# Kernel optimization log

Hardware: AMD Instinct MI355X
Metric: run time of the kernel (lower is better)

## Reference

```python
import jax, jax.numpy as jnp
import numpy as np

N_NODES = 100000
N_EDGES = 1600000
N_GRAPHS = 64
F = 128  # feature_dim == hidden_dim == embedding_dim
NUM_CONVS = 3


def _layernorm(h, g, b, eps=1e-5):
    mu = jnp.mean(h, axis=-1, keepdims=True)
    var = jnp.var(h, axis=-1, keepdims=True)
    return (h - mu) * jax.lax.rsqrt(var + eps) * g + b


def setup_inputs() -> dict:
    key = jax.random.key(0)
    ks = jax.random.split(key, 12)
    s = 1.0 / np.sqrt(F)
    return {
        "x": jax.random.normal(ks[0], (N_NODES, F), jnp.float32),
        "edge_index": jax.random.randint(ks[1], (2, N_EDGES), 0, N_NODES, jnp.int32),
        "batch_vec": jnp.sort(jax.random.randint(ks[2], (N_NODES,), 0, N_GRAPHS, jnp.int32)),
        "gammas": 1.0 + 0.1 * jax.random.normal(ks[3], (N_GRAPHS, NUM_CONVS), jnp.float32),
        "betas": 0.1 * jax.random.normal(ks[4], (N_GRAPHS, NUM_CONVS), jnp.float32),
        "pre_W0": s * jax.random.normal(ks[5], (F, F), jnp.float32),
        "pre_b0": jnp.zeros((F,), jnp.float32),
        "pre_W1": s * jax.random.normal(ks[6], (F, F), jnp.float32),
        "pre_b1": jnp.zeros((F,), jnp.float32),
        "gin_W": s * jax.random.normal(ks[7], (NUM_CONVS, 2, F, F), jnp.float32),
        "gin_b": jnp.zeros((NUM_CONVS, 2, F), jnp.float32),
        "post_W0": (1.0 / np.sqrt(5 * F)) * jax.random.normal(ks[8], (5 * F, F), jnp.float32),
        "post_b0": jnp.zeros((F,), jnp.float32),
        "post_ln_g": jnp.ones((F,), jnp.float32),
        "post_ln_b": jnp.zeros((F,), jnp.float32),
        "post_W1": s * jax.random.normal(ks[9], (F, F), jnp.float32),
        "post_b1": jnp.zeros((F,), jnp.float32),
    }


def reference(x, edge_index, batch_vec, gammas, betas,
              pre_W0, pre_b0, pre_W1, pre_b1,
              gin_W, gin_b,
              post_W0, post_b0, post_ln_g, post_ln_b, post_W1, post_b1):
    n = x.shape[0]
    src, dst = edge_index[0], edge_index[1]

    # preprocess MLP (2 layers, ReLU between, batch_norm='none')
    h = jnp.dot(jax.nn.relu(jnp.dot(x, pre_W0) + pre_b0), pre_W1) + pre_b1
    jump_xs = [x, h]

    # per-node FiLM coefficients (repeat_interleave over sorted batch == gather)
    g_nodes = gammas[batch_vec]  # [N, num_convs]
    b_nodes = betas[batch_vec]   # [N, num_convs]

    for i in range(NUM_CONVS):
        # GINConv, eps=0: MLP(h_i + sum_{j->i} h_j)
        aggr = jax.ops.segment_sum(h[src], dst, num_segments=n)
        z = h + aggr
        h = jnp.dot(jax.nn.relu(jnp.dot(z, gin_W[i, 0]) + gin_b[i, 0]), gin_W[i, 1]) + gin_b[i, 1]
        # FiLM modulation
        h = h * g_nodes[:, i:i + 1] + b_nodes[:, i:i + 1]
        jump_xs.append(h)

    # jumping knowledge 'cat'
    h = jnp.concatenate(jump_xs, axis=-1)  # [N, feature + 4*hidden]

    # postprocess MLP with LayerNorm (batch_norm='layer'); dropout p=0 (eval)
    z = jnp.dot(h, post_W0) + post_b0
    z = jax.nn.relu(_layernorm(z, post_ln_g, post_ln_b))
    return jnp.dot(z, post_W1) + post_b1
```

## Files before the change

### kernel.cpp

```cpp
#include <hip/hip_runtime.h>
#include <stdint.h>

#define FDIM 128
constexpr int EP_NONE = 0, EP_RELU = 1, EP_FILM = 2, EP_LNRELU = 3;

typedef __attribute__((ext_vector_type(8))) short short8v;
typedef __attribute__((ext_vector_type(4))) float f32x4;

struct Srcs { const float* p[5]; };
struct WPtrs { const float* p[14]; };

__device__ inline short f2bf(float f) {
  unsigned u = __float_as_uint(f);
  u = (u + 0x7fffu + ((u >> 16) & 1u)) >> 16;
  return (short)u;
}
__device__ inline float bf2f(short s) {
  return __uint_as_float(((unsigned)(unsigned short)s) << 16);
}


__global__ __launch_bounds__(256)
void k_hist(const int* __restrict__ dst, int* __restrict__ cnt, int E) {
  int e = blockIdx.x * 256 + threadIdx.x;
  if (e < E) atomicAdd(&cnt[dst[e]], 1);
}

__global__ __launch_bounds__(1024)
void k_scan_block(const int* __restrict__ cnt, int* __restrict__ scanned,
                  int* __restrict__ partials, int n) {
  __shared__ int sd[1024];
  int tid = threadIdx.x;
  int i = blockIdx.x * 1024 + tid;
  int v = (i < n) ? cnt[i] : 0;
  sd[tid] = v; __syncthreads();
  for (int off = 1; off < 1024; off <<= 1) {
    int t = (tid >= off) ? sd[tid - off] : 0;
    __syncthreads();
    sd[tid] += t;
    __syncthreads();
  }
  if (i < n) scanned[i] = sd[tid] - v;
  if (tid == 1023) partials[blockIdx.x] = sd[1023];
}

__global__ __launch_bounds__(128)
void k_scan_small(const int* __restrict__ partials, int* __restrict__ p2, int nb) {
  __shared__ int sd[128];
  int tid = threadIdx.x;
  int v = (tid < nb) ? partials[tid] : 0;
  sd[tid] = v; __syncthreads();
  for (int off = 1; off < 128; off <<= 1) {
    int t = (tid >= off) ? sd[tid - off] : 0;
    __syncthreads();
    sd[tid] += t;
    __syncthreads();
  }
  p2[tid] = sd[tid] - v;
}

__global__ __launch_bounds__(256)
void k_finalize(const int* __restrict__ scanned, const int* __restrict__ p2,
                int* __restrict__ indptr, int* __restrict__ cursor, int n, int E) {
  int i = blockIdx.x * 256 + threadIdx.x;
  if (i < n) {
    int v = scanned[i] + p2[i >> 10];
    indptr[i] = v;
    cursor[i] = v;
  }
  if (i == 0) indptr[n] = E;
}

__global__ __launch_bounds__(256)
void k_scatter(const int* __restrict__ src, const int* __restrict__ dst,
               int* __restrict__ cursor, int* __restrict__ eids, int E) {
  int e = blockIdx.x * 256 + threadIdx.x;
  if (e < E) {
    int p = atomicAdd(&cursor[dst[e]], 1);
    eids[p] = src[e];
  }
}


__global__ __launch_bounds__(256)
void k_aggr(const float* __restrict__ h, const int* __restrict__ indptr,
            const int* __restrict__ eids, float* __restrict__ z, int n) {
  int lane = threadIdx.x & 63;
  int node = blockIdx.x * 4 + (threadIdx.x >> 6);
  if (node >= n) return;
  float2 acc = *(const float2*)&h[(size_t)node * FDIM + lane * 2];
  int s = indptr[node], e = indptr[node + 1];
  for (int base = s; base < e; base += 64) {
    int cnt = min(64, e - base);
    int eid = (base + lane < e) ? eids[base + lane] : 0;
    int j = 0;
    for (; j + 4 <= cnt; j += 4) {
      int s0 = __shfl(eid, j, 64);
      int s1 = __shfl(eid, j + 1, 64);
      int s2 = __shfl(eid, j + 2, 64);
      int s3 = __shfl(eid, j + 3, 64);
      float2 v0 = *(const float2*)&h[(size_t)s0 * FDIM + lane * 2];
      float2 v1 = *(const float2*)&h[(size_t)s1 * FDIM + lane * 2];
      float2 v2 = *(const float2*)&h[(size_t)s2 * FDIM + lane * 2];
      float2 v3 = *(const float2*)&h[(size_t)s3 * FDIM + lane * 2];
      acc.x += v0.x + v1.x + v2.x + v3.x;
      acc.y += v0.y + v1.y + v2.y + v3.y;
    }
    for (; j < cnt; ++j) {
      int sn = __shfl(eid, j, 64);
      float2 hv = *(const float2*)&h[(size_t)sn * FDIM + lane * 2];
      acc.x += hv.x; acc.y += hv.y;
    }
  }
  *(float2*)&z[(size_t)node * FDIM + lane * 2] = acc;
}


__global__ __launch_bounds__(256)
void k_wt(WPtrs wp, short* __restrict__ wtHi, short* __restrict__ wtLo) {
  const int m = blockIdx.x;
  const float* __restrict__ W = wp.p[m];
  const int t = threadIdx.x;
  #pragma unroll
  for (int u = 0; u < 8; ++u) {
    int chunk = t + u * 256;
    int c = chunk >> 4, kc = chunk & 15;
    short8v hi, lo;
    #pragma unroll
    for (int j = 0; j < 8; ++j) {
      float w = W[(kc * 8 + j) * FDIM + c];
      short h = f2bf(w);
      hi[j] = h;
      lo[j] = f2bf(w - bf2f(h));
    }
    int off = m * 16384 + c * FDIM + kc * 8;
    *(short8v*)(wtHi + off) = hi;
    *(short8v*)(wtLo + off) = lo;
  }
}


template<int NSRC, int EPI>
__global__ __launch_bounds__(256)
void k_mfma(Srcs srcs, const short* __restrict__ wtHi, const short* __restrict__ wtLo,
            int m0, const float* __restrict__ bias, float* __restrict__ out, int n,
            const int* __restrict__ bvec, const float* __restrict__ gam,
            const float* __restrict__ bet, int conv,
            const float* __restrict__ lng, const float* __restrict__ lnb) {
  const int tid = threadIdx.x;
  const int lane = tid & 63;
  const int w = tid >> 6;
  const int lr = lane & 15;
  const int lg = lane >> 4;
  const int row0 = blockIdx.x * 128 + w * 32;

  f32x4 acc[2][8];
  #pragma unroll
  for (int s = 0; s < 2; ++s)
    #pragma unroll
    for (int f = 0; f < 8; ++f) acc[s][f] = (f32x4){0.f, 0.f, 0.f, 0.f};

  for (int js = 0; js < NSRC; ++js) {
    const float* __restrict__ A = srcs.p[js];
    const int wbase = (m0 + js) * 16384;
    #pragma unroll
    for (int k0i = 0; k0i < 4; ++k0i) {
      const int k0 = k0i * 32;
      short8v ah[2], al[2];
      #pragma unroll
      for (int s = 0; s < 2; ++s) {
        const int r = row0 + s * 16 + lr;
        float4 v0 = {0.f, 0.f, 0.f, 0.f}, v1 = {0.f, 0.f, 0.f, 0.f};
        if (r < n) {
          const float* Ar = A + (size_t)r * FDIM + k0 + lg * 8;
          v0 = *(const float4*)Ar;
          v1 = *(const float4*)(Ar + 4);
        }
        const float vv[8] = {v0.x, v0.y, v0.z, v0.w, v1.x, v1.y, v1.z, v1.w};
        #pragma unroll
        for (int j = 0; j < 8; ++j) {
          short h = f2bf(vv[j]);
          ah[s][j] = h;
          al[s][j] = f2bf(vv[j] - bf2f(h));
        }
      }
      #pragma unroll
      for (int f = 0; f < 8; ++f) {
        const int boff = wbase + (f * 16 + lr) * FDIM + k0 + lg * 8;
        short8v bh = *(const short8v*)(wtHi + boff);
        short8v bl = *(const short8v*)(wtLo + boff);
        acc[0][f] = __builtin_amdgcn_mfma_f32_16x16x32_bf16(ah[0], bh, acc[0][f], 0, 0, 0);
        acc[1][f] = __builtin_amdgcn_mfma_f32_16x16x32_bf16(ah[1], bh, acc[1][f], 0, 0, 0);
        acc[0][f] = __builtin_amdgcn_mfma_f32_16x16x32_bf16(al[0], bh, acc[0][f], 0, 0, 0);
        acc[1][f] = __builtin_amdgcn_mfma_f32_16x16x32_bf16(al[1], bh, acc[1][f], 0, 0, 0);
        acc[0][f] = __builtin_amdgcn_mfma_f32_16x16x32_bf16(ah[0], bl, acc[0][f], 0, 0, 0);
        acc[1][f] = __builtin_amdgcn_mfma_f32_16x16x32_bf16(ah[1], bl, acc[1][f], 0, 0, 0);
      }
    }
  }

  float bb[8];
  #pragma unroll
  for (int f = 0; f < 8; ++f) bb[f] = bias[f * 16 + lr];

  if constexpr (EPI == EP_LNRELU) {
    float gg[8], bn[8];
    #pragma unroll
    for (int f = 0; f < 8; ++f) { gg[f] = lng[f * 16 + lr]; bn[f] = lnb[f * 16 + lr]; }
    #pragma unroll
    for (int s = 0; s < 2; ++s) {
      float sm[4] = {0.f, 0.f, 0.f, 0.f}, sq[4] = {0.f, 0.f, 0.f, 0.f};
      #pragma unroll
      for (int f = 0; f < 8; ++f)
        #pragma unroll
        for (int i = 0; i < 4; ++i) {
          float v = acc[s][f][i] + bb[f];
          acc[s][f][i] = v;
          sm[i] += v; sq[i] += v * v;
        }
      #pragma unroll
      for (int m = 1; m < 16; m <<= 1)
        #pragma unroll
        for (int i = 0; i < 4; ++i) {
          sm[i] += __shfl_xor(sm[i], m, 64);
          sq[i] += __shfl_xor(sq[i], m, 64);
        }
      #pragma unroll
      for (int i = 0; i < 4; ++i) {
        const int r = row0 + s * 16 + 4 * lg + i;
        const float mu = sm[i] * (1.f / FDIM);
        const float var = sq[i] * (1.f / FDIM) - mu * mu;
        const float rs = rsqrtf(var + 1e-5f);
        if (r < n) {
          #pragma unroll
          for (int f = 0; f < 8; ++f) {
            float o = fmaxf((acc[s][f][i] - mu) * rs * gg[f] + bn[f], 0.f);
            out[(size_t)r * FDIM + f * 16 + lr] = o;
          }
        }
      }
    }
  } else {
    #pragma unroll
    for (int s = 0; s < 2; ++s)
      #pragma unroll
      for (int i = 0; i < 4; ++i) {
        const int r = row0 + s * 16 + 4 * lg + i;
        if (r >= n) continue;
        float g = 1.f, be = 0.f;
        if constexpr (EPI == EP_FILM) {
          int b = bvec[r];
          g = gam[b * 3 + conv];
          be = bet[b * 3 + conv];
        }
        #pragma unroll
        for (int f = 0; f < 8; ++f) {
          float o = acc[s][f][i] + bb[f];
          if constexpr (EPI == EP_RELU) o = fmaxf(o, 0.f);
          if constexpr (EPI == EP_FILM) o = o * g + be;
          out[(size_t)r * FDIM + f * 16 + lr] = o;
        }
      }
  }
}


extern "C" void kernel_launch(void* const* d_in, const int* in_sizes, int n_in,
                              void* d_out, int out_size, void* d_ws, size_t ws_size,
                              hipStream_t stream) {
  const float* x       = (const float*)d_in[0];
  const int*   eidx    = (const int*)d_in[1];
  const int*   bvec    = (const int*)d_in[2];
  const float* gam     = (const float*)d_in[3];
  const float* bet     = (const float*)d_in[4];
  const float* pre_W0  = (const float*)d_in[5];
  const float* pre_b0  = (const float*)d_in[6];
  const float* pre_W1  = (const float*)d_in[7];
  const float* pre_b1  = (const float*)d_in[8];
  const float* gin_W   = (const float*)d_in[9];
  const float* gin_b   = (const float*)d_in[10];
  const float* post_W0 = (const float*)d_in[11];
  const float* post_b0 = (const float*)d_in[12];
  const float* lng     = (const float*)d_in[13];
  const float* lnb     = (const float*)d_in[14];
  const float* post_W1 = (const float*)d_in[15];
  const float* post_b1 = (const float*)d_in[16];

  const int n = in_sizes[0] / FDIM;
  const int E = in_sizes[1] / 2;
  const int* esrc = eidx;
  const int* edst = eidx + E;
  float* out = (float*)d_out;

  const size_t NF = (size_t)n * FDIM;
  float* fws = (float*)d_ws;
  float* h0  = fws;
  float* h1  = fws + NF;
  float* h2  = fws + 2 * NF;
  float* h3  = fws + 3 * NF;
  float* zb  = out;
  float* tmp = out;
  int* iws      = (int*)(fws + 4 * NF);
  int* counts   = iws;
  int* scanned  = iws + n;
  int* indptr   = iws + 2 * n;
  int* cursor   = iws + 3 * n + 1;
  int* partials = iws + 4 * n + 1;
  int* p2       = partials + 128;
  int* eids     = p2 + 128;
  uintptr_t wtb = ((uintptr_t)(eids + E) + 15) & ~(uintptr_t)15;
  short* wtHi = (short*)wtb;
  short* wtLo = wtHi + 14 * 16384;

  WPtrs wp;
  wp.p[0] = pre_W0;
  wp.p[1] = pre_W1;
  for (int i = 0; i < 6; ++i) wp.p[2 + i] = gin_W + (size_t)i * 16384;
  for (int j = 0; j < 5; ++j) wp.p[8 + j] = post_W0 + (size_t)j * 16384;
  wp.p[13] = post_W1;
  k_wt<<<14, 256, 0, stream>>>(wp, wtHi, wtLo);

  hipMemsetAsync(counts, 0, (size_t)n * sizeof(int), stream);
  k_hist<<<(E + 255) / 256, 256, 0, stream>>>(edst, counts, E);
  const int nb = (n + 1023) / 1024;
  k_scan_block<<<nb, 1024, 0, stream>>>(counts, scanned, partials, n);
  k_scan_small<<<1, 128, 0, stream>>>(partials, p2, nb);
  k_finalize<<<(n + 255) / 256, 256, 0, stream>>>(scanned, p2, indptr, cursor, n, E);
  k_scatter<<<(E + 255) / 256, 256, 0, stream>>>(esrc, edst, cursor, eids, E);

  const int gb = (n + 127) / 128;

  Srcs sx{{x, nullptr, nullptr, nullptr, nullptr}};
  k_mfma<1, EP_RELU><<<gb, 256, 0, stream>>>(sx, wtHi, wtLo, 0, pre_b0, tmp, n,
                                             nullptr, nullptr, nullptr, 0, nullptr, nullptr);
  Srcs st0{{tmp, nullptr, nullptr, nullptr, nullptr}};
  k_mfma<1, EP_NONE><<<gb, 256, 0, stream>>>(st0, wtHi, wtLo, 1, pre_b1, h0, n,
                                             nullptr, nullptr, nullptr, 0, nullptr, nullptr);

  float* hprev = h0;
  float* houts[3] = {h1, h2, h3};
  for (int i = 0; i < 3; ++i) {
    k_aggr<<<(n + 3) / 4, 256, 0, stream>>>(hprev, indptr, eids, zb, n);
    Srcs sz{{zb, nullptr, nullptr, nullptr, nullptr}};
    k_mfma<1, EP_RELU><<<gb, 256, 0, stream>>>(
        sz, wtHi, wtLo, 2 + 2 * i, gin_b + (size_t)(2 * i) * FDIM, tmp, n,
        nullptr, nullptr, nullptr, 0, nullptr, nullptr);
    Srcs st{{tmp, nullptr, nullptr, nullptr, nullptr}};
    k_mfma<1, EP_FILM><<<gb, 256, 0, stream>>>(
        st, wtHi, wtLo, 3 + 2 * i, gin_b + (size_t)(2 * i + 1) * FDIM, houts[i], n,
        bvec, gam, bet, i, nullptr, nullptr);
    hprev = houts[i];
  }

  Srcs sj{{x, h0, h1, h2, h3}};
  k_mfma<5, EP_LNRELU><<<gb, 256, 0, stream>>>(sj, wtHi, wtLo, 8, post_b0, tmp, n,
                                               nullptr, nullptr, nullptr, 0, lng, lnb);
  Srcs sf{{tmp, nullptr, nullptr, nullptr, nullptr}};
  k_mfma<1, EP_NONE><<<gb, 256, 0, stream>>>(sf, wtHi, wtLo, 13, post_b1, out, n,
                                             nullptr, nullptr, nullptr, 0, nullptr, nullptr);
}
```

Before: 1.403 ms.

## Fuse two-layer MLPs into one kernel via LDS-staged hidden activations

Each pair of back-to-back GEMMs (pre-MLP, each GIN MLP, post-MLP) becomes a single kernel. The hidden activation is written as packed hi/lo bf16 into a swizzled 64KB LDS tile and never goes through global memory, which removes five launches and their intermediate write/read traffic. Source panels are also double-buffered in registers so loads overlap compute, and the aggregation loop is unrolled to 8 gathers. The cost is 64KB of LDS per block and heavier register pressure, which limits occupancy.

After: 1.412 ms. Within noise of the previous version (+0.7%).

```diff
diff --git a/kernel.cpp b/kernel.cpp
--- a/kernel.cpp
+++ b/kernel.cpp
@@ -6,16 +6,17 @@
 
 typedef __attribute__((ext_vector_type(8))) short short8v;
 typedef __attribute__((ext_vector_type(4))) float f32x4;
+typedef __attribute__((ext_vector_type(4))) unsigned int u32x4;
 
 struct Srcs { const float* p[5]; };
 struct WPtrs { const float* p[14]; };
 
-__device__ inline short f2bf(float f) {
+__device__ __forceinline__ short f2bf(float f) {
   unsigned u = __float_as_uint(f);
   u = (u + 0x7fffu + ((u >> 16) & 1u)) >> 16;
   return (short)u;
 }
-__device__ inline float bf2f(short s) {
+__device__ __forceinline__ float bf2f(short s) {
   return __uint_as_float(((unsigned)(unsigned short)s) << 16);
 }
 
@@ -94,17 +95,15 @@
     int cnt = min(64, e - base);
     int eid = (base + lane < e) ? eids[base + lane] : 0;
     int j = 0;
-    for (; j + 4 <= cnt; j += 4) {
-      int s0 = __shfl(eid, j, 64);
-      int s1 = __shfl(eid, j + 1, 64);
-      int s2 = __shfl(eid, j + 2, 64);
-      int s3 = __shfl(eid, j + 3, 64);
-      float2 v0 = *(const float2*)&h[(size_t)s0 * FDIM + lane * 2];
-      float2 v1 = *(const float2*)&h[(size_t)s1 * FDIM + lane * 2];
-      float2 v2 = *(const float2*)&h[(size_t)s2 * FDIM + lane * 2];
-      float2 v3 = *(const float2*)&h[(size_t)s3 * FDIM + lane * 2];
-      acc.x += v0.x + v1.x + v2.x + v3.x;
-      acc.y += v0.y + v1.y + v2.y + v3.y;
+    for (; j + 8 <= cnt; j += 8) {
+      float2 v[8];
+      #pragma unroll
+      for (int t = 0; t < 8; ++t) {
+        int sn = __shfl(eid, j + t, 64);
+        v[t] = *(const float2*)&h[(size_t)sn * FDIM + lane * 2];
+      }
+      #pragma unroll
+      for (int t = 0; t < 8; ++t) { acc.x += v[t].x; acc.y += v[t].y; }
     }
     for (; j < cnt; ++j) {
       int sn = __shfl(eid, j, 64);
@@ -140,13 +139,65 @@
 }
 
 
-template<int NSRC, int EPI>
-__global__ __launch_bounds__(256)
-void k_mfma(Srcs srcs, const short* __restrict__ wtHi, const short* __restrict__ wtLo,
-            int m0, const float* __restrict__ bias, float* __restrict__ out, int n,
-            const int* __restrict__ bvec, const float* __restrict__ gam,
-            const float* __restrict__ bet, int conv,
-            const float* __restrict__ lng, const float* __restrict__ lnb) {
+__device__ __forceinline__ void load_panel(float4 (&P)[2][4][2], const float* __restrict__ A,
+                                           int row0, int lr, int lg, int n) {
+  const float4 f4z = {0.f, 0.f, 0.f, 0.f};
+  #pragma unroll
+  for (int s = 0; s < 2; ++s) {
+    const int r = row0 + s * 16 + lr;
+    const bool ok = r < n;
+    const float* Ar = A + (size_t)r * FDIM + lg * 8;
+    #pragma unroll
+    for (int k = 0; k < 4; ++k) {
+      P[s][k][0] = ok ? *(const float4*)(Ar + k * 32) : f4z;
+      P[s][k][1] = ok ? *(const float4*)(Ar + k * 32 + 4) : f4z;
+    }
+  }
+}
+
+__device__ __forceinline__ void compute_panel(const float4 (&P)[2][4][2], f32x4 (&acc)[2][8],
+                                              const short* __restrict__ wtHi,
+                                              const short* __restrict__ wtLo,
+                                              int wbase, int lr, int lg) {
+  #pragma unroll
+  for (int k = 0; k < 4; ++k) {
+    short8v ah[2], al[2];
+    #pragma unroll
+    for (int s = 0; s < 2; ++s) {
+      const float vv[8] = {P[s][k][0].x, P[s][k][0].y, P[s][k][0].z, P[s][k][0].w,
+                           P[s][k][1].x, P[s][k][1].y, P[s][k][1].z, P[s][k][1].w};
+      #pragma unroll
+      for (int j = 0; j < 8; ++j) {
+        short h = f2bf(vv[j]);
+        ah[s][j] = h;
+        al[s][j] = f2bf(vv[j] - bf2f(h));
+      }
+    }
+    #pragma unroll
+    for (int f = 0; f < 8; ++f) {
+      const int boff = wbase + (f * 16 + lr) * FDIM + k * 32 + lg * 8;
+      short8v bh = *(const short8v*)(wtHi + boff);
+      short8v bl = *(const short8v*)(wtLo + boff);
+      acc[0][f] = __builtin_amdgcn_mfma_f32_16x16x32_bf16(ah[0], bh, acc[0][f], 0, 0, 0);
+      acc[1][f] = __builtin_amdgcn_mfma_f32_16x16x32_bf16(ah[1], bh, acc[1][f], 0, 0, 0);
+      acc[0][f] = __builtin_amdgcn_mfma_f32_16x16x32_bf16(al[0], bh, acc[0][f], 0, 0, 0);
+      acc[1][f] = __builtin_amdgcn_mfma_f32_16x16x32_bf16(al[1], bh, acc[1][f], 0, 0, 0);
+      acc[0][f] = __builtin_amdgcn_mfma_f32_16x16x32_bf16(ah[0], bl, acc[0][f], 0, 0, 0);
+      acc[1][f] = __builtin_amdgcn_mfma_f32_16x16x32_bf16(ah[1], bl, acc[1][f], 0, 0, 0);
+    }
+  }
+}
+
+template<int NSRC, int EPI1, int EPI2>
+__global__ __launch_bounds__(256, 2)
+void k_mlp(Srcs srcs, const short* __restrict__ wtHi, const short* __restrict__ wtLo,
+           int m0, int m1, const float* __restrict__ b1, const float* __restrict__ b2,
+           float* __restrict__ out, int n,
+           const int* __restrict__ bvec, const float* __restrict__ gam,
+           const float* __restrict__ bet, int conv,
+           const float* __restrict__ lng, const float* __restrict__ lnb) {
+  __shared__ unsigned int lds[128 * FDIM];
+
   const int tid = threadIdx.x;
   const int lane = tid & 63;
   const int w = tid >> 6;
@@ -160,87 +211,123 @@
     #pragma unroll
     for (int f = 0; f < 8; ++f) acc[s][f] = (f32x4){0.f, 0.f, 0.f, 0.f};
 
-  for (int js = 0; js < NSRC; ++js) {
-    const float* __restrict__ A = srcs.p[js];
-    const int wbase = (m0 + js) * 16384;
-    #pragma unroll
-    for (int k0i = 0; k0i < 4; ++k0i) {
-      const int k0 = k0i * 32;
-      short8v ah[2], al[2];
-      #pragma unroll
-      for (int s = 0; s < 2; ++s) {
-        const int r = row0 + s * 16 + lr;
-        float4 v0 = {0.f, 0.f, 0.f, 0.f}, v1 = {0.f, 0.f, 0.f, 0.f};
-        if (r < n) {
-          const float* Ar = A + (size_t)r * FDIM + k0 + lg * 8;
-          v0 = *(const float4*)Ar;
-          v1 = *(const float4*)(Ar + 4);
+  float4 P0[2][4][2], P1[2][4][2];
+  load_panel(P0, srcs.p[0], row0, lr, lg, n);
+  if constexpr (NSRC >= 2) load_panel(P1, srcs.p[1], row0, lr, lg, n);
+  compute_panel(P0, acc, wtHi, wtLo, (m0 + 0) * 16384, lr, lg);
+  if constexpr (NSRC >= 3) load_panel(P0, srcs.p[2], row0, lr, lg, n);
+  if constexpr (NSRC >= 2) compute_panel(P1, acc, wtHi, wtLo, (m0 + 1) * 16384, lr, lg);
+  if constexpr (NSRC >= 4) load_panel(P1, srcs.p[3], row0, lr, lg, n);
+  if constexpr (NSRC >= 3) compute_panel(P0, acc, wtHi, wtLo, (m0 + 2) * 16384, lr, lg);
+  if constexpr (NSRC >= 5) load_panel(P0, srcs.p[4], row0, lr, lg, n);
+  if constexpr (NSRC >= 4) compute_panel(P1, acc, wtHi, wtLo, (m0 + 3) * 16384, lr, lg);
+  if constexpr (NSRC >= 5) compute_panel(P0, acc, wtHi, wtLo, (m0 + 4) * 16384, lr, lg);
+
+  {
+    float bb[8];
+    #pragma unroll
+    for (int f = 0; f < 8; ++f) bb[f] = b1[f * 16 + lr];
+    #pragma unroll
+    for (int s = 0; s < 2; ++s) {
+      #pragma unroll
+      for (int f = 0; f < 8; ++f)
+        #pragma unroll
+        for (int i = 0; i < 4; ++i) acc[s][f][i] += bb[f];
+
+      if constexpr (EPI1 == EP_LNRELU) {
+        float sm[4] = {0.f, 0.f, 0.f, 0.f}, sq[4] = {0.f, 0.f, 0.f, 0.f};
+        #pragma unroll
+        for (int f = 0; f < 8; ++f)
+          #pragma unroll
+          for (int i = 0; i < 4; ++i) {
+            float v = acc[s][f][i];
+            sm[i] += v; sq[i] += v * v;
+          }
+        #pragma unroll
+        for (int m = 1; m < 16; m <<= 1)
+          #pragma unroll
+          for (int i = 0; i < 4; ++i) {
+            sm[i] += __shfl_xor(sm[i], m, 64);
+            sq[i] += __shfl_xor(sq[i], m, 64);
+          }
+        float gg[8], bn[8];
+        #pragma unroll
+        for (int f = 0; f < 8; ++f) { gg[f] = lng[f * 16 + lr]; bn[f] = lnb[f * 16 + lr]; }
+        #pragma unroll
+        for (int i = 0; i < 4; ++i) {
+          const float mu = sm[i] * (1.f / FDIM);
+          const float var = sq[i] * (1.f / FDIM) - mu * mu;
+          const float rs = rsqrtf(var + 1e-5f);
+          #pragma unroll
+          for (int f = 0; f < 8; ++f)
+            acc[s][f][i] = fmaxf((acc[s][f][i] - mu) * rs * gg[f] + bn[f], 0.f);
         }
-        const float vv[8] = {v0.x, v0.y, v0.z, v0.w, v1.x, v1.y, v1.z, v1.w};
-        #pragma unroll
-        for (int j = 0; j < 8; ++j) {
-          short h = f2bf(vv[j]);
-          ah[s][j] = h;
-          al[s][j] = f2bf(vv[j] - bf2f(h));
+      } else {
+        #pragma unroll
+        for (int f = 0; f < 8; ++f)
+          #pragma unroll
+          for (int i = 0; i < 4; ++i) acc[s][f][i] = fmaxf(acc[s][f][i], 0.f);
+      }
+
+      #pragma unroll
+      for (int f = 0; f < 8; ++f)
+        #pragma unroll
+        for (int i = 0; i < 4; ++i) {
+          float v = acc[s][f][i];
+          short hi = f2bf(v);
+          short lo = f2bf(v - bf2f(hi));
+          unsigned pk = (unsigned)(unsigned short)hi | ((unsigned)(unsigned short)lo << 16);
+          const int rl = w * 32 + s * 16 + 4 * lg + i;
+          const int c = f * 16 + lr;
+          lds[rl * FDIM + (c ^ ((rl & 7) * 8))] = pk;
         }
+    }
+  }
+  __syncthreads();
+
+  f32x4 acc2[2][8];
+  #pragma unroll
+  for (int s = 0; s < 2; ++s)
+    #pragma unroll
+    for (int f = 0; f < 8; ++f) acc2[s][f] = (f32x4){0.f, 0.f, 0.f, 0.f};
+
+  const int wbase2 = m1 * 16384;
+  #pragma unroll
+  for (int k = 0; k < 4; ++k) {
+    short8v ah[2], al[2];
+    #pragma unroll
+    for (int s = 0; s < 2; ++s) {
+      const int rl = w * 32 + s * 16 + lr;
+      const int kidx = k * 32 + lg * 8;
+      const int idx = rl * FDIM + (kidx ^ ((rl & 7) * 8));
+      u32x4 u0 = *(const u32x4*)&lds[idx];
+      u32x4 u1 = *(const u32x4*)&lds[idx + 4];
+      #pragma unroll
+      for (int j = 0; j < 4; ++j) {
+        ah[s][j]     = (short)(u0[j] & 0xffffu);
+        al[s][j]     = (short)(u0[j] >> 16);
+        ah[s][j + 4] = (short)(u1[j] & 0xffffu);
+        al[s][j + 4] = (short)(u1[j] >> 16);
       }
-      #pragma unroll
-      for (int f = 0; f < 8; ++f) {
-        const int boff = wbase + (f * 16 + lr) * FDIM + k0 + lg * 8;
-        short8v bh = *(const short8v*)(wtHi + boff);
-        short8v bl = *(const short8v*)(wtLo + boff);
-        acc[0][f] = __builtin_amdgcn_mfma_f32_16x16x32_bf16(ah[0], bh, acc[0][f], 0, 0, 0);
-        acc[1][f] = __builtin_amdgcn_mfma_f32_16x16x32_bf16(ah[1], bh, acc[1][f], 0, 0, 0);
-        acc[0][f] = __builtin_amdgcn_mfma_f32_16x16x32_bf16(al[0], bh, acc[0][f], 0, 0, 0);
-        acc[1][f] = __builtin_amdgcn_mfma_f32_16x16x32_bf16(al[1], bh, acc[1][f], 0, 0, 0);
-        acc[0][f] = __builtin_amdgcn_mfma_f32_16x16x32_bf16(ah[0], bl, acc[0][f], 0, 0, 0);
-        acc[1][f] = __builtin_amdgcn_mfma_f32_16x16x32_bf16(ah[1], bl, acc[1][f], 0, 0, 0);
-      }
-    }
-  }
-
-  float bb[8];
-  #pragma unroll
-  for (int f = 0; f < 8; ++f) bb[f] = bias[f * 16 + lr];
-
-  if constexpr (EPI == EP_LNRELU) {
-    float gg[8], bn[8];
-    #pragma unroll
-    for (int f = 0; f < 8; ++f) { gg[f] = lng[f * 16 + lr]; bn[f] = lnb[f * 16 + lr]; }
-    #pragma unroll
-    for (int s = 0; s < 2; ++s) {
-      float sm[4] = {0.f, 0.f, 0.f, 0.f}, sq[4] = {0.f, 0.f, 0.f, 0.f};
-      #pragma unroll
-      for (int f = 0; f < 8; ++f)
-        #pragma unroll
-        for (int i = 0; i < 4; ++i) {
-          float v = acc[s][f][i] + bb[f];
-          acc[s][f][i] = v;
-          sm[i] += v; sq[i] += v * v;
-        }
-      #pragma unroll
-      for (int m = 1; m < 16; m <<= 1)
-        #pragma unroll
-        for (int i = 0; i < 4; ++i) {
-          sm[i] += __shfl_xor(sm[i], m, 64);
-          sq[i] += __shfl_xor(sq[i], m, 64);
-        }
-      #pragma unroll
-      for (int i = 0; i < 4; ++i) {
-        const int r = row0 + s * 16 + 4 * lg + i;
-        const float mu = sm[i] * (1.f / FDIM);
-        const float var = sq[i] * (1.f / FDIM) - mu * mu;
-        const float rs = rsqrtf(var + 1e-5f);
-        if (r < n) {
-          #pragma unroll
-          for (int f = 0; f < 8; ++f) {
-            float o = fmaxf((acc[s][f][i] - mu) * rs * gg[f] + bn[f], 0.f);
-            out[(size_t)r * FDIM + f * 16 + lr] = o;
-          }
-        }
-      }
-    }
-  } else {
+    }
+    #pragma unroll
+    for (int f = 0; f < 8; ++f) {
+      const int boff = wbase2 + (f * 16 + lr) * FDIM + k * 32 + lg * 8;
+      short8v bh = *(const short8v*)(wtHi + boff);
+      short8v bl = *(const short8v*)(wtLo + boff);
+      acc2[0][f] = __builtin_amdgcn_mfma_f32_16x16x32_bf16(ah[0], bh, acc2[0][f], 0, 0, 0);
+      acc2[1][f] = __builtin_amdgcn_mfma_f32_16x16x32_bf16(ah[1], bh, acc2[1][f], 0, 0, 0);
+      acc2[0][f] = __builtin_amdgcn_mfma_f32_16x16x32_bf16(al[0], bh, acc2[0][f], 0, 0, 0);
+      acc2[1][f] = __builtin_amdgcn_mfma_f32_16x16x32_bf16(al[1], bh, acc2[1][f], 0, 0, 0);
+      acc2[0][f] = __builtin_amdgcn_mfma_f32_16x16x32_bf16(ah[0], bl, acc2[0][f], 0, 0, 0);
+      acc2[1][f] = __builtin_amdgcn_mfma_f32_16x16x32_bf16(ah[1], bl, acc2[1][f], 0, 0, 0);
+    }
+  }
+
+  {
+    float bb[8];
+    #pragma unroll
+    for (int f = 0; f < 8; ++f) bb[f] = b2[f * 16 + lr];
     #pragma unroll
     for (int s = 0; s < 2; ++s)
       #pragma unroll
@@ -248,16 +335,15 @@
         const int r = row0 + s * 16 + 4 * lg + i;
         if (r >= n) continue;
         float g = 1.f, be = 0.f;
-        if constexpr (EPI == EP_FILM) {
+        if constexpr (EPI2 == EP_FILM) {
           int b = bvec[r];
           g = gam[b * 3 + conv];
           be = bet[b * 3 + conv];
         }
         #pragma unroll
         for (int f = 0; f < 8; ++f) {
-          float o = acc[s][f][i] + bb[f];
-          if constexpr (EPI == EP_RELU) o = fmaxf(o, 0.f);
-          if constexpr (EPI == EP_FILM) o = o * g + be;
+          float o = acc2[s][f][i] + bb[f];
+          if constexpr (EPI2 == EP_FILM) o = o * g + be;
           out[(size_t)r * FDIM + f * 16 + lr] = o;
         }
       }
@@ -299,7 +385,6 @@
   float* h2  = fws + 2 * NF;
   float* h3  = fws + 3 * NF;
   float* zb  = out;
-  float* tmp = out;
   int* iws      = (int*)(fws + 4 * NF);
   int* counts   = iws;
   int* scanned  = iws + n;
@@ -331,31 +416,24 @@
   const int gb = (n + 127) / 128;
 
   Srcs sx{{x, nullptr, nullptr, nullptr, nullptr}};
-  k_mfma<1, EP_RELU><<<gb, 256, 0, stream>>>(sx, wtHi, wtLo, 0, pre_b0, tmp, n,
-                                             nullptr, nullptr, nullptr, 0, nullptr, nullptr);
-  Srcs st0{{tmp, nullptr, nullptr, nullptr, nullptr}};
-  k_mfma<1, EP_NONE><<<gb, 256, 0, stream>>>(st0, wtHi, wtLo, 1, pre_b1, h0, n,
-                                             nullptr, nullptr, nullptr, 0, nullptr, nullptr);
+  k_mlp<1, EP_RELU, EP_NONE><<<gb, 256, 0, stream>>>(
+      sx, wtHi, wtLo, 0, 1, pre_b0, pre_b1, h0, n,
+      nullptr, nullptr, nullptr, 0, nullptr, nullptr);
 
   float* hprev = h0;
   float* houts[3] = {h1, h2, h3};
   for (int i = 0; i < 3; ++i) {
     k_aggr<<<(n + 3) / 4, 256, 0, stream>>>(hprev, indptr, eids, zb, n);
     Srcs sz{{zb, nullptr, nullptr, nullptr, nullptr}};
-    k_mfma<1, EP_RELU><<<gb, 256, 0, stream>>>(
-        sz, wtHi, wtLo, 2 + 2 * i, gin_b + (size_t)(2 * i) * FDIM, tmp, n,
-        nullptr, nullptr, nullptr, 0, nullptr, nullptr);
-    Srcs st{{tmp, nullptr, nullptr, nullptr, nullptr}};
-    k_mfma<1, EP_FILM><<<gb, 256, 0, stream>>>(
-        st, wtHi, wtLo, 3 + 2 * i, gin_b + (size_t)(2 * i + 1) * FDIM, houts[i], n,
-        bvec, gam, bet, i, nullptr, nullptr);
+    k_mlp<1, EP_RELU, EP_FILM><<<gb, 256, 0, stream>>>(
+        sz, wtHi, wtLo, 2 + 2 * i, 3 + 2 * i,
+        gin_b + (size_t)(2 * i) * FDIM, gin_b + (size_t)(2 * i + 1) * FDIM,
+        houts[i], n, bvec, gam, bet, i, nullptr, nullptr);
     hprev = houts[i];
   }
 
   Srcs sj{{x, h0, h1, h2, h3}};
-  k_mfma<5, EP_LNRELU><<<gb, 256, 0, stream>>>(sj, wtHi, wtLo, 8, post_b0, tmp, n,
-                                               nullptr, nullptr, nullptr, 0, lng, lnb);
-  Srcs sf{{tmp, nullptr, nullptr, nullptr, nullptr}};
-  k_mfma<1, EP_NONE><<<gb, 256, 0, stream>>>(sf, wtHi, wtLo, 13, post_b1, out, n,
-                                             nullptr, nullptr, nullptr, 0, nullptr, nullptr);
-}
+  k_mlp<5, EP_LNRELU, EP_NONE><<<gb, 256, 0, stream>>>(
+      sj, wtHi, wtLo, 8, 13, post_b0, post_b1, out, n,
+      nullptr, nullptr, nullptr, 0, lng, lnb);
+}
```
